# Optimization experiments

Hardware: AMD Instinct MI355X
Metric: run time of the kernel (lower is better)

The kernel has to match this reference:

```python
import jax, jax.numpy as jnp
import numpy as np

B, P, N0 = 8, 32, 10000
K, HIDP = 8, 4
HIDR = 4 * K * HIDP + K   # 136 = backbone output channels
HEADS = 2
E = 160000


def _conv_bn(x, w, b, g, be, dil):
    # x: [B,1,P,N0]; w: [k,1,ks,1]; valid conv along time with dilation dil, then BatchNorm2d (batch stats)
    y = jax.lax.conv_general_dilated(x, w, (1, 1), 'VALID', rhs_dilation=(dil, 1),
                                     dimension_numbers=('NCHW', 'OIHW', 'NCHW'))
    y = y + b[None, :, None, None]
    mu = jnp.mean(y, axis=(0, 2, 3), keepdims=True)
    var = jnp.var(y, axis=(0, 2, 3), keepdims=True)
    return g[None, :, None, None] * (y - mu) * jax.lax.rsqrt(var + 1e-5) + be[None, :, None, None]


def _branch(x, w, b, g, be, dil, pool):
    y = _conv_bn(x, w, b, g, be, dil)
    if pool:  # AdaptiveMaxPool2d((HIDP, N0)): pools only the time axis (node axis already N0)
        T = y.shape[2]
        y = jnp.stack([jnp.max(y[:, :, (i * T) // HIDP: -((-(i + 1) * T) // HIDP), :], axis=2)
                       for i in range(HIDP)], axis=2)
    return y.reshape(y.shape[0], -1, y.shape[-1])  # [B, k*hidP or k, N0]


def _backbone(x, pl1, pl2, pp1, pp2, pg):
    x = x.reshape(-1, 1, P, N0)
    parts = [_branch(x, *pl1, 1, True), _branch(x, *pl2, 1, True),   # local: ks 3,5 dil 1
             _branch(x, *pp1, 2, True), _branch(x, *pp2, 2, True),   # periodic: ks 3,5 dil 2
             _branch(x, *pg, 1, False)]                               # global: ks P, no pool
    return jnp.tanh(jnp.concatenate(parts, axis=1).transpose(0, 2, 1))  # [B, N0, HIDR]


def _gat(xn, W, a_src, a_dst, bias, src, dst, heads, out_ch):
    # PyG GATConv: linear (no bias) -> per-head additive attention -> segment softmax over dst -> scatter-sum
    n = xn.shape[0]
    h = (xn @ W).reshape(n, heads, out_ch)                              # [N,H,C]
    al = jax.nn.leaky_relu(jnp.sum(h * a_src, -1)[src] + jnp.sum(h * a_dst, -1)[dst], 0.2)  # [E',H]
    amax = jax.ops.segment_max(al, dst, num_segments=n)
    ex = jnp.exp(al - amax[dst])
    coef = ex / (jax.ops.segment_sum(ex, dst, num_segments=n)[dst] + 1e-16)
    out = jax.ops.segment_sum(coef[:, :, None] * h[src], dst, num_segments=n)  # [N,H,C]
    return out.reshape(n, heads * out_ch) + bias


def setup_inputs() -> dict:
    key = jax.random.key(0)
    ks = iter(jax.random.split(key, 64))
    nrm = lambda *s: jax.random.normal(next(ks), s, jnp.float32) * 0.05
    d = {"x": jax.random.normal(next(ks), (B, P, N0), jnp.float32)}
    for nm, ksz in (("l1", 3), ("l2", 5), ("p1", 3), ("p2", 5), ("g", P)):
        d["w_" + nm] = nrm(K, 1, ksz, 1)
        d["b_" + nm] = nrm(K)
        d["g_" + nm] = jnp.ones((K,), jnp.float32)
        d["be_" + nm] = jnp.zeros((K,), jnp.float32)
    d["W1"] = nrm(HIDR, HEADS * HIDR); d["as1"] = nrm(HEADS, HIDR); d["ad1"] = nrm(HEADS, HIDR); d["bb1"] = nrm(HEADS * HIDR)
    d["W2"] = nrm(HEADS * HIDR, HIDR); d["as2"] = nrm(1, HIDR); d["ad2"] = nrm(1, HIDR); d["bb2"] = nrm(HIDR)
    d["Wo"] = nrm(2 * HIDR, HIDR); d["bo"] = nrm(HIDR)
    d["Wo2"] = nrm(HIDR, 1); d["bo2"] = nrm(1)
    d["edge_index"] = jax.random.randint(next(ks), (2, E), 0, N0, jnp.int32)
    return d


def reference(x, w_l1, b_l1, g_l1, be_l1, w_l2, b_l2, g_l2, be_l2,
              w_p1, b_p1, g_p1, be_p1, w_p2, b_p2, g_p2, be_p2,
              w_g, b_g, g_g, be_g,
              W1, as1, ad1, bb1, W2, as2, ad2, bb2, Wo, bo, Wo2, bo2, edge_index):
    feat = _backbone(x, (w_l1, b_l1, g_l1, be_l1), (w_l2, b_l2, g_l2, be_l2),
                     (w_p1, b_p1, g_p1, be_p1), (w_p2, b_p2, g_p2, be_p2),
                     (w_g, b_g, g_g, be_g))                                  # [B,N0,HIDR]
    loop = jnp.arange(N0, dtype=edge_index.dtype)                            # GATConv add_self_loops=True
    src = jnp.concatenate([edge_index[0], loop])
    dst = jnp.concatenate([edge_index[1], loop])
    # original loops GATConv per batch item over shared edge_index; vmap is the batched equivalent
    g1 = jax.vmap(lambda f: _gat(f, W1, as1, ad1, bb1, src, dst, HEADS, HIDR))(feat)  # [B,N0,2*HIDR]
    g2 = jax.vmap(lambda f: _gat(f, W2, as2, ad2, bb2, src, dst, 1, HIDR))(g1)        # [B,N0,HIDR]
    ns = jax.nn.leaky_relu(jnp.concatenate([g2, feat], axis=-1))             # dropout is identity at eval
    res = jax.nn.leaky_relu(ns @ Wo + bo)
    return (res @ Wo2 + bo2)[..., 0]                                         # [B,N0]
```

## Files before the change

kernel.cpp:

```cpp
#include <hip/hip_runtime.h>
#include <hip/hip_bf16.h>
#include <math.h>

typedef unsigned short u16;
typedef unsigned int   u32;
typedef short v8s __attribute__((ext_vector_type(8)));
typedef float v4f __attribute__((ext_vector_type(4)));
typedef float v2f __attribute__((ext_vector_type(2)));
#define DEV static __device__ __forceinline__

DEV float u2f(u16 u){ union{u32 i; float f;} v; v.i = ((u32)u)<<16; return v.f; }
DEV u16   f2u(float f){ union{float ff; u32 i;} v; v.ff = f; u32 r = v.i + 0x7fffu + ((v.i>>16)&1u); return (u16)(r>>16); }
DEV float lrelu02(float x){ return x > 0.f ? x : 0.2f*x; }
DEV float lrelu01(float x){ return x > 0.f ? x : 0.01f*x; }
DEV float fast_tanh(float x){
  float cx = fminf(fmaxf(x, -15.f), 15.f);
  float e = __expf(2.f*cx);
  return (e - 1.f) * __builtin_amdgcn_rcpf(e + 1.f);
}
DEV float wred_sum(float v){
  #pragma unroll
  for (int o = 32; o > 0; o >>= 1) v += __shfl_xor(v, o, 64);
  return v;
}
DEV float wred_max32(float v){
  #pragma unroll
  for (int o = 16; o > 0; o >>= 1) v = fmaxf(v, __shfl_xor(v, o, 64));
  return v;
}
DEV float wred_sum32(float v){
  #pragma unroll
  for (int o = 16; o > 0; o >>= 1) v += __shfl_xor(v, o, 64);
  return v;
}
DEV v2f unpack2(u32 w){
  v2f r;
  r.x = __uint_as_float(w << 16);
  r.y = __uint_as_float(w & 0xffff0000u);
  return r;
}

constexpr int B_   = 8;
constexpr int P_   = 32;
constexpr int N0_  = 10000;
constexpr int NODES = B_ * N0_;
constexpr int E_   = 160000;
constexpr int NE_  = E_ + N0_;

__global__ void __launch_bounds__(256) k_setup(int* __restrict__ zbase,
    const float* __restrict__ Wo, u16* __restrict__ WoT,
    const float* __restrict__ W1, const float* __restrict__ W2, u16* __restrict__ W12T,
    const float* __restrict__ as1, const float* __restrict__ ad1,
    float* __restrict__ va1s, float* __restrict__ va1d,
    const float* __restrict__ as2, const float* __restrict__ ad2,
    const float* __restrict__ bb1,
    float* __restrict__ v2ss, float* __restrict__ v2dd,
    float* __restrict__ cc, float* __restrict__ b12)
{
  __shared__ float l2s[272], l2d[272];
  int blk = blockIdx.x, tid = threadIdx.x;
  if (blk < 79){ int i = blk*256 + tid; if (i < 20080) zbase[i] = 0; return; }
  blk -= 79;
  if (blk < 180){
    int i = blk*256 + tid; if (i >= 144*320) return;
    int n = i/320, k = i - n*320; float v = 0.f;
    if (n < 136){
      if (k < 136) v = Wo[(size_t)k*136 + n];
      else if (k >= 160 && k < 296) v = Wo[(size_t)(k-24)*136 + n];
    }
    WoT[i] = f2u(v); return;
  }
  blk -= 180;
  if (blk < 162){
    int i = blk*256 + tid; if (i >= 144*288) return;
    int n = i/288, kk = i - n*288; float v = 0.f;
    if (n < 136 && kk < 272){
      int hh = kk/136, k = kk - hh*136;
      for (int c = 0; c < 136; c++)
        v = fmaf(W1[(size_t)k*272 + hh*136 + c], W2[(size_t)(hh*136+c)*136 + n], v);
    }
    W12T[i] = f2u(v); return;
  }
  blk -= 162;
  if (blk < 2){
    int t = blk*256 + tid; if (t >= 272) return;
    int hh = t/136, k = t - hh*136; float s = 0.f, d = 0.f;
    for (int c = 0; c < 136; c++){
      float w = W1[(size_t)k*272 + hh*136 + c];
      s = fmaf(w, as1[hh*136+c], s);
      d = fmaf(w, ad1[hh*136+c], d);
    }
    va1s[t] = s; va1d[t] = d; return;
  }
  blk -= 2;
  {
    for (int m = tid; m < 272; m += 256){
      float vs = 0.f, vd = 0.f;
      for (int n2 = 0; n2 < 136; n2++){
        float w2 = W2[(size_t)m*136 + n2];
        vs = fmaf(w2, as2[n2], vs);
        vd = fmaf(w2, ad2[n2], vd);
      }
      l2s[m] = vs; l2d[m] = vd;
    }
    __syncthreads();
    int t0 = blk*256 + tid;
    if (t0 < 272){
      int hh = t0/136, k = t0 - hh*136; float s = 0.f, d = 0.f;
      for (int c = 0; c < 136; c++){
        float w = W1[(size_t)k*272 + hh*136 + c];
        s = fmaf(w, l2s[hh*136+c], s);
        d = fmaf(w, l2d[hh*136+c], d);
      }
      v2ss[t0] = s; v2dd[t0] = d;
    }
    if (blk == 1){
      if (tid < 64){
        float s = 0.f, d = 0.f;
        for (int m = tid; m < 272; m += 64){
          s = fmaf(bb1[m], l2s[m], s);
          d = fmaf(bb1[m], l2d[m], d);
        }
        s = wred_sum(s); d = wred_sum(d);
        if (tid == 0){ cc[0] = s; cc[1] = d; }
      } else if (tid < 200){
        int n2 = tid - 64; float v = 0.f;
        for (int m = 0; m < 272; m++) v = fmaf(bb1[m], W2[(size_t)m*136 + n2], v);
        b12[n2] = v;
      }
    }
  }
}

DEV void load_convw(float* lw, const float* wl1, const float* wl2, const float* wp1,
                    const float* wp2, const float* wg, int tid, int nth){
  for (int i = tid; i < 384; i += nth){
    float v;
    if      (i < 24)  v = wl1[i];
    else if (i < 64)  v = wl2[i-24];
    else if (i < 88)  v = wp1[i-64];
    else if (i < 128) v = wp2[i-88];
    else              v = wg [i-128];
    lw[i] = v;
  }
}

template<int KS,int DIL,int T>
DEV void conv_stats(const float* xc, const float* wk, float& s, float& q){
  #pragma unroll
  for (int t = 0; t < T; t++){
    float v = 0.f;
    #pragma unroll
    for (int j = 0; j < KS; j++) v = fmaf(wk[j], xc[t + j*DIL], v);
    s += v; q = fmaf(v, v, q);
  }
}

__global__ void __launch_bounds__(256) k_bn_stats(
    const float* __restrict__ x,
    const float* __restrict__ wl1, const float* __restrict__ wl2,
    const float* __restrict__ wp1, const float* __restrict__ wp2,
    const float* __restrict__ wg,
    float* __restrict__ gsum, float* __restrict__ gsq)
{
  __shared__ float lw[384];
  __shared__ float lacc[80];
  const int tid = threadIdx.x;
  load_convw(lw, wl1, wl2, wp1, wp2, wg, tid, 256);
  if (tid < 80) lacc[tid] = 0.f;
  __syncthreads();

  const int lane = tid & 63, wv = tid >> 6;
  const int nodeLocal = (wv >> 1)*64 + lane;
  const int half = wv & 1;
  const int gid = blockIdx.x*128 + nodeLocal;
  float xc[P_];
  if (gid < NODES){
    int b = gid / N0_, n = gid - b*N0_;
    const float* xp = x + (size_t)b*P_*N0_ + n;
    #pragma unroll
    for (int p = 0; p < P_; p++) xc[p] = xp[(size_t)p*N0_];
  } else {
    #pragma unroll
    for (int p = 0; p < P_; p++) xc[p] = 0.f;
  }

  auto red = [&](int ch, float s, float q){
    #pragma unroll
    for (int o = 32; o > 0; o >>= 1){ s += __shfl_down(s,o,64); q += __shfl_down(q,o,64); }
    if (lane == 0){ atomicAdd(&lacc[ch], s); atomicAdd(&lacc[40+ch], q); }
  };

  if (half == 0){
    #pragma unroll
    for (int k = 0; k < 8; k++){ float s=0,q=0; conv_stats<3,1,30>(xc, lw      + k*3 , s,q); red(k,     s,q); }
    #pragma unroll
    for (int k = 0; k < 8; k++){ float s=0,q=0; conv_stats<5,1,28>(xc, lw + 24 + k*5 , s,q); red(8+k,   s,q); }
  } else {
    #pragma unroll
    for (int k = 0; k < 8; k++){ float s=0,q=0; conv_stats<3,2,28>(xc, lw + 64 + k*3 , s,q); red(16+k,  s,q); }
    #pragma unroll
    for (int k = 0; k < 8; k++){ float s=0,q=0; conv_stats<5,2,24>(xc, lw + 88 + k*5 , s,q); red(24+k,  s,q); }
    #pragma unroll
    for (int k = 0; k < 8; k++){ float s=0,q=0; conv_stats<32,1,1>(xc, lw + 128+ k*32, s,q); red(32+k,  s,q); }
  }

  __syncthreads();
  if (tid < 40)      atomicAdd(&gsum[tid],    lacc[tid]);
  else if (tid < 80) atomicAdd(&gsq [tid-40], lacc[tid]);
}

__global__ void k_count(const int* __restrict__ ei, int* __restrict__ counts,
                        const float* __restrict__ gsum, const float* __restrict__ gsq,
                        float* __restrict__ sA, float* __restrict__ sB,
                        const float* g0, const float* g1, const float* g2, const float* g3, const float* g4,
                        const float* e0, const float* e1, const float* e2, const float* e3, const float* e4){
  if (blockIdx.x == 665){
    int t = threadIdx.x;
    if (t >= 40) return;
    int bi = t >> 3, k = t & 7;
    const int Ts[5] = {30,28,28,24,1};
    float cnt  = (float)NODES * (float)Ts[bi];
    float mean = gsum[t] / cnt;
    float var  = gsq[t] / cnt - mean*mean;
    const float* gp = bi==0?g0: bi==1?g1: bi==2?g2: bi==3?g3: g4;
    const float* ep = bi==0?e0: bi==1?e1: bi==2?e2: bi==3?e3: e4;
    float a = gp[k] * rsqrtf(fmaxf(var, 0.f) + 1e-5f);
    sA[t] = a;
    sB[t] = ep[k] - a*mean;
    return;
  }
  int e = blockIdx.x*blockDim.x + threadIdx.x;
  if (e >= NE_) return;
  int dst = (e < E_) ? ei[E_ + e] : (e - E_);
  atomicAdd(&counts[dst], 1);
}

__global__ void __launch_bounds__(1024) k_scan_perm(const int* __restrict__ counts,
                                                    int* __restrict__ offs,
                                                    int* __restrict__ perm){
  __shared__ int part[1024];
  __shared__ int hist[129];
  __shared__ int base[129];
  int t = threadIdx.x;
  if (blockIdx.x == 0){
    int loc[10]; int s = 0;
    #pragma unroll
    for (int i = 0; i < 10; i++){
      int idx = t*10 + i;
      int c = (idx < N0_) ? counts[idx] : 0;
      loc[i] = s; s += c;
    }
    part[t] = s;
    __syncthreads();
    for (int o = 1; o < 1024; o <<= 1){
      int v = (t >= o) ? part[t-o] : 0;
      __syncthreads();
      part[t] += v;
      __syncthreads();
    }
    int pre = (t == 0) ? 0 : part[t-1];
    #pragma unroll
    for (int i = 0; i < 10; i++){
      int idx = t*10 + i;
      if (idx < N0_) offs[idx] = pre + loc[i];
    }
    if (t == 0) offs[N0_] = part[1023];
  } else {
    if (t < 129) hist[t] = 0;
    __syncthreads();
    int dloc[10];
    #pragma unroll
    for (int i = 0; i < 10; i++){
      int idx = t*10 + i;
      if (idx < N0_){
        int d = min(counts[idx], 128);
        dloc[i] = d;
        atomicAdd(&hist[d], 1);
      }
    }
    __syncthreads();
    if (t == 0){
      int s = 0;
      for (int b = 0; b <= 128; b++){ base[b] = s; s += hist[b]; }
    }
    __syncthreads();
    #pragma unroll
    for (int i = 0; i < 10; i++){
      int idx = t*10 + i;
      if (idx < N0_){
        int pos = atomicAdd(&base[dloc[i]], 1);
        perm[pos] = idx;
      }
    }
  }
}

__global__ void k_scatter(const int* __restrict__ ei, const int* __restrict__ offs,
                          int* __restrict__ cursor, int* __restrict__ srcl){
  int e = blockIdx.x*blockDim.x + threadIdx.x;
  if (e >= NE_) return;
  int src, dst;
  if (e < E_){ src = ei[e]; dst = ei[E_ + e]; } else { src = dst = e - E_; }
  int pos = atomicAdd(&cursor[dst], 1);
  srcl[offs[dst] + pos] = src;
}

template<int KS,int DIL,int T>
DEV void conv_pool4(const float* xc, const float* wk, float A, float Bc, float* o4){
  float y[T];
  #pragma unroll
  for (int t = 0; t < T; t++){
    float v = 0.f;
    #pragma unroll
    for (int j = 0; j < KS; j++) v = fmaf(wk[j], xc[t + j*DIL], v);
    y[t] = fmaf(A, v, Bc);
  }
  #pragma unroll
  for (int i = 0; i < 4; i++){
    const int lo = (i*T)/4, hi = ((i+1)*T + 3)/4;
    float m = y[lo];
    #pragma unroll
    for (int t = 0; t < T; t++){ if (t > lo && t < hi) m = fmaxf(m, y[t]); }
    o4[i] = m;
  }
}

__global__ void __launch_bounds__(256) k_feat(
    const float* __restrict__ x,
    const float* __restrict__ wl1, const float* __restrict__ wl2,
    const float* __restrict__ wp1, const float* __restrict__ wp2,
    const float* __restrict__ wg,
    const float* __restrict__ sA, const float* __restrict__ sB,
    const float* __restrict__ va1s, const float* __restrict__ va1d,
    u16* __restrict__ feat, u16* __restrict__ featL,
    float* __restrict__ asrc1, float* __restrict__ adst1,
    int base, int m)
{
  __shared__ float lw[384];
  __shared__ float lA[40], lB[40];
  __shared__ float4 lv4[136];
  __shared__ float sdt[128][4];
  const int tid = threadIdx.x;
  load_convw(lw, wl1, wl2, wp1, wp2, wg, tid, 256);
  if (tid < 40){ lA[tid] = sA[tid]; lB[tid] = sB[tid]; }
  for (int i = tid; i < 136; i += 256)
    lv4[i] = make_float4(va1s[i], va1d[i], va1s[136+i], va1d[136+i]);
  __syncthreads();

  const int lane = tid & 63, wv = tid >> 6;
  const int nodeLocal = (wv >> 1)*64 + lane;
  const int half = wv & 1;
  const int nodeIdx = blockIdx.x*128 + nodeLocal;
  const bool act = nodeIdx < m;
  const int gcl = base + (act ? nodeIdx : (m-1));
  int b = gcl / N0_, n = gcl - b*N0_;
  float xc[P_];
  const float* xp = x + (size_t)b*P_*N0_ + n;
  #pragma unroll
  for (int p = 0; p < P_; p++) xc[p] = xp[(size_t)p*N0_];

  float dt[4] = {0.f,0.f,0.f,0.f};
  u32 pk[4], pkl[4];
  u16* orow  = feat  + (size_t)nodeIdx*160;
  u16* olrow = featL + (size_t)nodeIdx*160;
  auto emit = [&](int ch, float v){
    float t = fast_tanh(v);
    float4 vv = lv4[ch];
    dt[0] = fmaf(t, vv.x, dt[0]);
    dt[1] = fmaf(t, vv.y, dt[1]);
    dt[2] = fmaf(t, vv.z, dt[2]);
    dt[3] = fmaf(t, vv.w, dt[3]);
    u16 h  = f2u(t);
    u16 hl = f2u(lrelu01(t));
    int s = ch & 7;
    if ((s & 1) == 0){ pk[s>>1] = h;                pkl[s>>1] = hl; }
    else             { pk[s>>1] |= ((u32)h) << 16;  pkl[s>>1] |= ((u32)hl) << 16; }
    if (s == 7 && act){
      *(uint4*)(orow  + (ch - 7)) = make_uint4(pk[0],pk[1],pk[2],pk[3]);
      *(uint4*)(olrow + (ch - 7)) = make_uint4(pkl[0],pkl[1],pkl[2],pkl[3]);
    }
  };

  float o4[4];
  if (half == 0){
    #pragma unroll
    for (int k = 0; k < 8; k++){
      conv_pool4<3,1,30>(xc, lw + k*3, lA[k], lB[k], o4);
      #pragma unroll
      for (int i = 0; i < 4; i++) emit(k*4+i, o4[i]);
    }
    #pragma unroll
    for (int k = 0; k < 8; k++){
      conv_pool4<5,1,28>(xc, lw + 24 + k*5, lA[8+k], lB[8+k], o4);
      #pragma unroll
      for (int i = 0; i < 4; i++) emit(32 + k*4+i, o4[i]);
    }
  } else {
    #pragma unroll
    for (int k = 0; k < 8; k++){
      conv_pool4<3,2,28>(xc, lw + 64 + k*3, lA[16+k], lB[16+k], o4);
      #pragma unroll
      for (int i = 0; i < 4; i++) emit(64 + k*4+i, o4[i]);
    }
    #pragma unroll
    for (int k = 0; k < 8; k++){
      conv_pool4<5,2,24>(xc, lw + 88 + k*5, lA[24+k], lB[24+k], o4);
      #pragma unroll
      for (int i = 0; i < 4; i++) emit(96 + k*4+i, o4[i]);
    }
    #pragma unroll
    for (int k = 0; k < 8; k++){
      float v = 0.f;
      #pragma unroll
      for (int j = 0; j < 32; j++) v = fmaf(lw[128 + k*32 + j], xc[j], v);
      emit(128 + k, fmaf(lA[32+k], v, lB[32+k]));
    }
  }

  if (half == 1){
    sdt[nodeLocal][0] = dt[0]; sdt[nodeLocal][1] = dt[1];
    sdt[nodeLocal][2] = dt[2]; sdt[nodeLocal][3] = dt[3];
  }
  __syncthreads();
  if (half == 0 && act){
    asrc1[(size_t)nodeIdx*2]   = dt[0] + sdt[nodeLocal][0];
    asrc1[(size_t)nodeIdx*2+1] = dt[2] + sdt[nodeLocal][2];
    adst1[(size_t)nodeIdx*2]   = dt[1] + sdt[nodeLocal][1];
    adst1[(size_t)nodeIdx*2+1] = dt[3] + sdt[nodeLocal][3];
  }
}

template<int MT,int KT1,int KT2,int NT,int EPI,int LR2>
__global__ void __launch_bounds__(256) k_mfma(
    const u16* __restrict__ A1, int sA1,
    const u16* __restrict__ A2, int sA2,
    const u16* __restrict__ BT, int sBT,
    u16* __restrict__ C, int sC, int nbase,
    const float* __restrict__ bias, int m,
    const float* __restrict__ w2v, const float* __restrict__ bo2p, float* __restrict__ fout)
{
  const int wv = threadIdx.x >> 6, lane = threadIdx.x & 63;
  const int quad = lane >> 4, l15 = lane & 15;
  const int mb = blockIdx.x*(MT*64) + wv*(MT*16);
  int ar[MT];
  #pragma unroll
  for (int mt = 0; mt < MT; mt++) ar[mt] = min(mb + mt*16 + l15, m-1);

  v4f acc[MT][NT];
  #pragma unroll
  for (int mt = 0; mt < MT; mt++)
    #pragma unroll
    for (int nt = 0; nt < NT; nt++)
      acc[mt][nt] = (v4f){0.f,0.f,0.f,0.f};

  for (int kt = 0; kt < KT1+KT2; kt++){
    const u16* ab; int sA, koff;
    if (KT2 == 0 || kt < KT1){ ab = A1; sA = sA1; koff = kt*32; }
    else { ab = A2; sA = sA2; koff = (kt-KT1)*32; }
    v8s a[MT];
    #pragma unroll
    for (int mt = 0; mt < MT; mt++)
      a[mt] = *(const v8s*)(ab + (size_t)ar[mt]*sA + koff + quad*8);
    if (KT2 > 0 && LR2 && kt >= KT1){
      #pragma unroll
      for (int mt = 0; mt < MT; mt++)
        #pragma unroll
        for (int j = 0; j < 8; j++){
          float f = u2f((u16)a[mt][j]);
          f = f > 0.f ? f : 0.01f*f;
          a[mt][j] = (short)f2u(f);
        }
    }
    const int kb = kt*32 + quad*8;
    #pragma unroll
    for (int nt = 0; nt < NT; nt++){
      v8s b = *(const v8s*)(BT + (size_t)(nbase + nt*16 + l15)*sBT + kb);
      #pragma unroll
      for (int mt = 0; mt < MT; mt++)
        acc[mt][nt] = __builtin_amdgcn_mfma_f32_16x16x32_bf16(a[mt], b, acc[mt][nt], 0, 0, 0);
    }
  }

  if (EPI == 2){
    const float bo2v = bo2p[0];
    #pragma unroll
    for (int mt = 0; mt < MT; mt++){
      float part[4] = {0.f,0.f,0.f,0.f};
      #pragma unroll
      for (int nt = 0; nt < NT; nt++){
        const int col = nt*16 + l15;
        float wv2 = (col < 136) ? w2v[col] : 0.f;
        float bv  = bias[min(col,135)];
        #pragma unroll
        for (int i = 0; i < 4; i++){
          float xv = lrelu01(acc[mt][nt][i] + bv);
          part[i] = fmaf(xv, wv2, part[i]);
        }
      }
      #pragma unroll
      for (int i = 0; i < 4; i++){
        float v = part[i];
        v += __shfl_xor(v, 1, 64);
        v += __shfl_xor(v, 2, 64);
        v += __shfl_xor(v, 4, 64);
        v += __shfl_xor(v, 8, 64);
        int r = mb + mt*16 + quad*4 + i;
        if (l15 == 0 && r < m) fout[r] = v + bo2v;
      }
    }
    return;
  }

  #pragma unroll
  for (int mt = 0; mt < MT; mt++){
    const int r0 = mb + mt*16 + quad*4;
    #pragma unroll
    for (int nt = 0; nt < NT; nt++){
      const int col = nbase + nt*16 + l15;
      #pragma unroll
      for (int i = 0; i < 4; i++){
        int r = r0 + i;
        if (r < m){
          float xv = acc[mt][nt][i];
          if (EPI == 1){ xv += bias[min(col,135)]; xv = lrelu01(xv); }
          if (EPI == 3){ xv += bias[min(col,135)]; }
          C[(size_t)r*sC + col] = f2u(xv);
        }
      }
    }
  }
}

__global__ void __launch_bounds__(256) k_agg1(const u16* __restrict__ feat,
    const float* __restrict__ asrc, const float* __restrict__ adst,
    const int* __restrict__ offs, const int* __restrict__ srcl,
    const int* __restrict__ perm,
    u16* __restrict__ aggF,
    const float* __restrict__ v2s, const float* __restrict__ v2d,
    const float* __restrict__ cc,
    float* __restrict__ as_out, float* __restrict__ ad_out,
    int cbMask, int cbShift)
{
  __shared__ int4 smeta[4][2][32];
  const int tid = threadIdx.x;
  const int wv = tid >> 6, lane = tid & 63;
  const int half = lane >> 5, l32 = lane & 31;
  const int id = blockIdx.x;
  const int bb = id & cbMask;
  const int q = (id >> cbShift)*4 + wv;
  const int dst = perm[2*q + half];
  const int nbase = bb*N0_;
  const int node = nbase + dst;
  const int start = offs[dst], end = offs[dst+1];
  const int ne = end - start;

  const float ad0 = adst[(size_t)node*2], ad1v = adst[(size_t)node*2+1];
  const char* featB = (const char*)feat;

  v2f m01h0 = {0.f,0.f}, m23h0 = {0.f,0.f};
  v2f m01h1 = {0.f,0.f}, m23h1 = {0.f,0.f};
  v2f r01h0 = {0.f,0.f}, r01h1 = {0.f,0.f};

  auto acc_one = [&](int4 mt){
    const u16* fp = (const u16*)(featB + mt.x);
    float c0 = __int_as_float(mt.y), c1 = __int_as_float(mt.z);
    const uint2 hv = *(const uint2*)(fp + 4*l32);
    v2f f01 = unpack2(hv.x), f23 = unpack2(hv.y);
    v2f cc0 = {c0,c0}, cc1 = {c1,c1};
    m01h0 = __builtin_elementwise_fma(f01, cc0, m01h0);
    m23h0 = __builtin_elementwise_fma(f23, cc0, m23h0);
    m01h1 = __builtin_elementwise_fma(f01, cc1, m01h1);
    m23h1 = __builtin_elementwise_fma(f23, cc1, m23h1);
    if (l32 < 4){
      const u32 hr = *(const u32*)(fp + 128 + 2*l32);
      v2f g01 = unpack2(hr);
      r01h0 = __builtin_elementwise_fma(g01, cc0, r01h0);
      r01h1 = __builtin_elementwise_fma(g01, cc1, r01h1);
    }
  };
  auto acc_four = [&](int4 ma, int4 mb, int4 mc, int4 md){
    const u16* p0 = (const u16*)(featB + ma.x);
    const u16* p1 = (const u16*)(featB + mb.x);
    const u16* p2 = (const u16*)(featB + mc.x);
    const u16* p3 = (const u16*)(featB + md.x);
    const uint2 v0 = *(const uint2*)(p0 + 4*l32);
    const uint2 v1 = *(const uint2*)(p1 + 4*l32);
    const uint2 v2 = *(const uint2*)(p2 + 4*l32);
    const uint2 v3 = *(const uint2*)(p3 + 4*l32);
    u32 q0, q1, q2, q3;
    if (l32 < 4){
      q0 = *(const u32*)(p0 + 128 + 2*l32);
      q1 = *(const u32*)(p1 + 128 + 2*l32);
      q2 = *(const u32*)(p2 + 128 + 2*l32);
      q3 = *(const u32*)(p3 + 128 + 2*l32);
    }
    v2f f01, f23, cA, cB;
    #define EDGE1(vv, qq, mm) \
      f01 = unpack2(vv.x); f23 = unpack2(vv.y); \
      cA = (v2f){__int_as_float(mm.y), __int_as_float(mm.y)}; \
      cB = (v2f){__int_as_float(mm.z), __int_as_float(mm.z)}; \
      m01h0 = __builtin_elementwise_fma(f01, cA, m01h0); \
      m23h0 = __builtin_elementwise_fma(f23, cA, m23h0); \
      m01h1 = __builtin_elementwise_fma(f01, cB, m01h1); \
      m23h1 = __builtin_elementwise_fma(f23, cB, m23h1); \
      if (l32 < 4){ \
        v2f g01 = unpack2(qq); \
        r01h0 = __builtin_elementwise_fma(g01, cA, r01h0); \
        r01h1 = __builtin_elementwise_fma(g01, cB, r01h1); \
      }
    EDGE1(v0, q0, ma)
    EDGE1(v1, q1, mb)
    EDGE1(v2, q2, mc)
    EDGE1(v3, q3, md)
    #undef EDGE1
  };
  auto run_chunk = [&](int cnt){
    const int4* mp = &smeta[wv][half][0];
    int j = 0;
    for (; j + 3 < cnt; j += 4)
      acc_four(mp[j], mp[j+1], mp[j+2], mp[j+3]);
    for (; j < cnt; j++)
      acc_one(mp[j]);
  };

  if (ne <= 32){
    const bool has = l32 < ne;
    const int sn = nbase + (has ? srcl[start + l32] : 0);
    const int offL = sn * 320;
    float al0 = has ? lrelu02(asrc[(size_t)sn*2]   + ad0)  : -1e30f;
    float al1 = has ? lrelu02(asrc[(size_t)sn*2+1] + ad1v) : -1e30f;
    float mm = wred_max32(al0);
    float p0 = has ? __expf(al0 - mm) : 0.f;
    float c0 = p0 * (1.f/(wred_sum32(p0) + 1e-16f));
    mm = wred_max32(al1);
    float p1 = has ? __expf(al1 - mm) : 0.f;
    float c1 = p1 * (1.f/(wred_sum32(p1) + 1e-16f));
    if (has)
      smeta[wv][half][l32] = make_int4(offL, __float_as_int(c0), __float_as_int(c1), 0);
    asm volatile("s_waitcnt lgkmcnt(0)" ::: "memory");
    run_chunk(ne);
  } else {
    float lm0 = -1e30f, lm1 = -1e30f;
    for (int e = start + l32; e < end; e += 32){
      int sn = nbase + srcl[e];
      lm0 = fmaxf(lm0, lrelu02(asrc[(size_t)sn*2]   + ad0));
      lm1 = fmaxf(lm1, lrelu02(asrc[(size_t)sn*2+1] + ad1v));
    }
    float m0 = wred_max32(lm0), m1 = wred_max32(lm1);
    float ls0 = 0.f, ls1 = 0.f;
    for (int e = start + l32; e < end; e += 32){
      int sn = nbase + srcl[e];
      ls0 += __expf(lrelu02(asrc[(size_t)sn*2]   + ad0)  - m0);
      ls1 += __expf(lrelu02(asrc[(size_t)sn*2+1] + ad1v) - m1);
    }
    float si0 = 1.f/(wred_sum32(ls0) + 1e-16f);
    float si1 = 1.f/(wred_sum32(ls1) + 1e-16f);
    for (int cs = start; cs < end; cs += 32){
      int cnt = min(32, end - cs);
      bool has = l32 < cnt;
      int sn = nbase + (has ? srcl[cs + l32] : 0);
      int offL = sn * 320;
      float c0 = 0.f, c1 = 0.f;
      if (has){
        c0 = __expf(lrelu02(asrc[(size_t)sn*2]   + ad0)  - m0) * si0;
        c1 = __expf(lrelu02(asrc[(size_t)sn*2+1] + ad1v) - m1) * si1;
      }
      if (has)
        smeta[wv][half][l32] = make_int4(offL, __float_as_int(c0), __float_as_int(c1), 0);
      asm volatile("s_waitcnt lgkmcnt(0)" ::: "memory");
      run_chunk(cnt);
    }
  }

  u16* outp = aggF + (size_t)node*288;
  {
    ushort4 s0; s0.x=f2u(m01h0.x); s0.y=f2u(m01h0.y); s0.z=f2u(m23h0.x); s0.w=f2u(m23h0.y);
    *(ushort4*)(outp + 4*l32) = s0;
    ushort4 s1; s1.x=f2u(m01h1.x); s1.y=f2u(m01h1.y); s1.z=f2u(m23h1.x); s1.w=f2u(m23h1.y);
    *(ushort4*)(outp + 136 + 4*l32) = s1;
    if (l32 < 4){
      ushort2 t0; t0.x=f2u(r01h0.x); t0.y=f2u(r01h0.y);
      *(ushort2*)(outp + 128 + 2*l32) = t0;
      ushort2 t1; t1.x=f2u(r01h1.x); t1.y=f2u(r01h1.y);
      *(ushort2*)(outp + 136 + 128 + 2*l32) = t1;
    }
  }
  {
    int c = 4*l32;
    float s = m01h0.x*v2s[c] + m01h0.y*v2s[c+1] + m23h0.x*v2s[c+2] + m23h0.y*v2s[c+3]
            + m01h1.x*v2s[136+c] + m01h1.y*v2s[136+c+1] + m23h1.x*v2s[136+c+2] + m23h1.y*v2s[136+c+3];
    float d = m01h0.x*v2d[c] + m01h0.y*v2d[c+1] + m23h0.x*v2d[c+2] + m23h0.y*v2d[c+3]
            + m01h1.x*v2d[136+c] + m01h1.y*v2d[136+c+1] + m23h1.x*v2d[136+c+2] + m23h1.y*v2d[136+c+3];
    if (l32 < 4){
      int cr = 128 + 2*l32;
      s += r01h0.x*v2s[cr] + r01h0.y*v2s[cr+1] + r01h1.x*v2s[136+cr] + r01h1.y*v2s[136+cr+1];
      d += r01h0.x*v2d[cr] + r01h0.y*v2d[cr+1] + r01h1.x*v2d[136+cr] + r01h1.y*v2d[136+cr+1];
    }
    s = wred_sum32(s); d = wred_sum32(d);
    if (l32 == 0){ as_out[node] = s + cc[0]; ad_out[node] = d + cc[1]; }
  }
}

__global__ void __launch_bounds__(256) k_agg2(const u16* __restrict__ h, int sh,
    const float* __restrict__ asrc, const float* __restrict__ adst,
    const int* __restrict__ offs, const int* __restrict__ srcl,
    const int* __restrict__ perm,
    const float* __restrict__ bias, u16* __restrict__ outp0, int so,
    int cbMask, int cbShift)
{
  __shared__ int2 smeta[4][2][32];
  const int tid = threadIdx.x;
  const int wv = tid >> 6, lane = tid & 63;
  const int half = lane >> 5, l32 = lane & 31;
  const int id = blockIdx.x;
  const int bb = id & cbMask;
  const int q = (id >> cbShift)*4 + wv;
  const int dst = perm[2*q + half];
  const int nbase = bb*N0_;
  const int node = nbase + dst;
  const int start = offs[dst], end = offs[dst+1];
  const int ne = end - start;
  const int bstride = 2*sh;

  const float adh = adst[node];
  const char* hB = (const char*)h;

  v2f a01 = {0.f,0.f}, a23 = {0.f,0.f}, r01 = {0.f,0.f};

  auto acc_one = [&](int2 mt){
    const u16* hp = (const u16*)(hB + mt.x);
    float c0 = __int_as_float(mt.y);
    const uint2 hv = *(const uint2*)(hp + 4*l32);
    v2f cc0 = {c0,c0};
    a01 = __builtin_elementwise_fma(unpack2(hv.x), cc0, a01);
    a23 = __builtin_elementwise_fma(unpack2(hv.y), cc0, a23);
    if (l32 < 4){
      const u32 hr = *(const u32*)(hp + 128 + 2*l32);
      r01 = __builtin_elementwise_fma(unpack2(hr), cc0, r01);
    }
  };
  auto acc_four = [&](int2 ma, int2 mb, int2 mc, int2 md){
    const u16* p0 = (const u16*)(hB + ma.x);
    const u16* p1 = (const u16*)(hB + mb.x);
    const u16* p2 = (const u16*)(hB + mc.x);
    const u16* p3 = (const u16*)(hB + md.x);
    const uint2 v0 = *(const uint2*)(p0 + 4*l32);
    const uint2 v1 = *(const uint2*)(p1 + 4*l32);
    const uint2 v2 = *(const uint2*)(p2 + 4*l32);
    const uint2 v3 = *(const uint2*)(p3 + 4*l32);
    u32 q0, q1, q2, q3;
    if (l32 < 4){
      q0 = *(const u32*)(p0 + 128 + 2*l32);
      q1 = *(const u32*)(p1 + 128 + 2*l32);
      q2 = *(const u32*)(p2 + 128 + 2*l32);
      q3 = *(const u32*)(p3 + 128 + 2*l32);
    }
    v2f cc;
    #define EDGE2(vv, qq, mm) \
      cc = (v2f){__int_as_float(mm.y), __int_as_float(mm.y)}; \
      a01 = __builtin_elementwise_fma(unpack2(vv.x), cc, a01); \
      a23 = __builtin_elementwise_fma(unpack2(vv.y), cc, a23); \
      if (l32 < 4) r01 = __builtin_elementwise_fma(unpack2(qq), cc, r01);
    EDGE2(v0, q0, ma)
    EDGE2(v1, q1, mb)
    EDGE2(v2, q2, mc)
    EDGE2(v3, q3, md)
    #undef EDGE2
  };
  auto run_chunk = [&](int cnt){
    const int2* mp = &smeta[wv][half][0];
    int j = 0;
    for (; j + 3 < cnt; j += 4)
      acc_four(mp[j], mp[j+1], mp[j+2], mp[j+3]);
    for (; j < cnt; j++)
      acc_one(mp[j]);
  };

  if (ne <= 32){
    const bool has = l32 < ne;
    const int sn = nbase + (has ? srcl[start + l32] : 0);
    const int offL = sn * bstride;
    float al = has ? lrelu02(asrc[sn] + adh) : -1e30f;
    float m = wred_max32(al);
    float p = has ? __expf(al - m) : 0.f;
    float c0 = p * (1.f/(wred_sum32(p) + 1e-16f));
    if (has)
      smeta[wv][half][l32] = make_int2(offL, __float_as_int(c0));
    asm volatile("s_waitcnt lgkmcnt(0)" ::: "memory");
    run_chunk(ne);
  } else {
    float lm = -1e30f;
    for (int e = start + l32; e < end; e += 32){
      int sn = nbase + srcl[e];
      lm = fmaxf(lm, lrelu02(asrc[sn] + adh));
    }
    float m = wred_max32(lm);
    float ls = 0.f;
    for (int e = start + l32; e < end; e += 32){
      int sn = nbase + srcl[e];
      ls += __expf(lrelu02(asrc[sn] + adh) - m);
    }
    float si = 1.f/(wred_sum32(ls) + 1e-16f);
    for (int cs = start; cs < end; cs += 32){
      int cnt = min(32, end - cs);
      bool has = l32 < cnt;
      int sn = nbase + (has ? srcl[cs + l32] : 0);
      int offL = sn * bstride;
      float c0 = has ? __expf(lrelu02(asrc[sn] + adh) - m) * si : 0.f;
      if (has)
        smeta[wv][half][l32] = make_int2(offL, __float_as_int(c0));
      asm volatile("s_waitcnt lgkmcnt(0)" ::: "memory");
      run_chunk(cnt);
    }
  }

  u16* outp = outp0 + (size_t)node*so;
  {
    int c = 4*l32;
    ushort4 st;
    st.x = f2u(lrelu01(a01.x + bias[c]));
    st.y = f2u(lrelu01(a01.y + bias[c+1]));
    st.z = f2u(lrelu01(a23.x + bias[c+2]));
    st.w = f2u(lrelu01(a23.y + bias[c+3]));
    *(ushort4*)(outp + c) = st;
    if (l32 < 4){
      int cr = 128 + 2*l32;
      ushort2 sr;
      sr.x = f2u(lrelu01(r01.x + bias[cr]));
      sr.y = f2u(lrelu01(r01.y + bias[cr+1]));
      *(ushort2*)(outp + cr) = sr;
    }
  }
}

extern "C" void kernel_launch(void* const* d_in, const int* in_sizes, int n_in,
                              void* d_out, int out_size, void* d_ws, size_t ws_size,
                              hipStream_t stream)
{
  (void)in_sizes; (void)n_in; (void)out_size;
  const float* x    = (const float*)d_in[0];
  const float* wl1  = (const float*)d_in[1];
  const float* gl1  = (const float*)d_in[3];
  const float* bel1 = (const float*)d_in[4];
  const float* wl2  = (const float*)d_in[5];
  const float* gl2  = (const float*)d_in[7];
  const float* bel2 = (const float*)d_in[8];
  const float* wp1  = (const float*)d_in[9];
  const float* gp1  = (const float*)d_in[11];
  const float* bep1 = (const float*)d_in[12];
  const float* wp2  = (const float*)d_in[13];
  const float* gp2  = (const float*)d_in[15];
  const float* bep2 = (const float*)d_in[16];
  const float* wg   = (const float*)d_in[17];
  const float* gg   = (const float*)d_in[19];
  const float* beg  = (const float*)d_in[20];
  const float* W1   = (const float*)d_in[21];
  const float* as1  = (const float*)d_in[22];
  const float* ad1  = (const float*)d_in[23];
  const float* bb1  = (const float*)d_in[24];
  const float* W2   = (const float*)d_in[25];
  const float* as2  = (const float*)d_in[26];
  const float* ad2  = (const float*)d_in[27];
  const float* bb2  = (const float*)d_in[28];
  const float* Wo   = (const float*)d_in[29];
  const float* bo   = (const float*)d_in[30];
  const float* Wo2  = (const float*)d_in[31];
  const float* bo2  = (const float*)d_in[32];
  const int*   ei   = (const int*)d_in[33];

  const size_t STATIC_BYTES = 1250000;
  int nc = 1;
  while (nc < 8 && STATIC_BYTES + (size_t)1880*(NODES/nc) > ws_size) nc <<= 1;
  const int CB = B_/nc, CN = CB*N0_;
  int cbShift = 0; while ((1 << cbShift) < CB) cbShift++;
  const int cbMask = CB - 1;

  char* wsb = (char*)d_ws; size_t off = 0;
  auto alloc = [&](size_t nbytes)->void*{
    void* p = wsb + off; off = (off + nbytes + 255) & ~(size_t)255; return p;
  };
  int*   zbase  = (int*)  alloc(20080*sizeof(int));
  float* gsum   = (float*)zbase;
  float* gsq    = gsum + 40;
  int*   counts = zbase + 80;
  int*   cursor = counts + 10000;
  float* sA     = (float*)alloc(40*sizeof(float));
  float* sB     = (float*)alloc(40*sizeof(float));
  int*   offs   = (int*)  alloc(10001*sizeof(int));
  int*   srcl   = (int*)  alloc((size_t)NE_*sizeof(int));
  int*   perm   = (int*)  alloc((size_t)N0_*sizeof(int));
  u16*   W12T   = (u16*)  alloc((size_t)144*288*2);
  u16*   WoT    = (u16*)  alloc((size_t)144*320*2);
  float* va1s   = (float*)alloc(272*sizeof(float));
  float* va1d   = (float*)alloc(272*sizeof(float));
  float* v2ss   = (float*)alloc(272*sizeof(float));
  float* v2dd   = (float*)alloc(272*sizeof(float));
  float* ccv    = (float*)alloc(2*sizeof(float));
  float* b12    = (float*)alloc(136*sizeof(float));
  u16*   feat   = (u16*)  alloc((size_t)CN*160*2);
  u16*   featL  = (u16*)  alloc((size_t)CN*160*2);
  u16*   aggF   = (u16*)  alloc((size_t)CN*288*2);
  u16*   h2     = (u16*)  alloc((size_t)CN*144*2);
  u16*   g2l    = (u16*)  alloc((size_t)CN*160*2);
  float* asrc1  = (float*)alloc((size_t)CN*2*sizeof(float));
  float* adst1  = (float*)alloc((size_t)CN*2*sizeof(float));
  float* asrc2  = (float*)alloc((size_t)CN*sizeof(float));
  float* adst2  = (float*)alloc((size_t)CN*sizeof(float));

  k_setup<<<425,256,0,stream>>>(zbase, Wo, WoT, W1, W2, W12T,
                                as1, ad1, va1s, va1d, as2, ad2, bb1,
                                v2ss, v2dd, ccv, b12);

  k_bn_stats<<<625,256,0,stream>>>(x, wl1,wl2,wp1,wp2,wg, gsum, gsq);

  k_count  <<<666,256,0,stream>>>(ei, counts, gsum, gsq, sA, sB,
                                  gl1,gl2,gp1,gp2,gg, bel1,bel2,bep1,bep2,beg);
  k_scan_perm<<<2,1024,0,stream>>>(counts, offs, perm);
  k_scatter<<<665,256,0,stream>>>(ei, offs, cursor, srcl);

  const int gxm = (CN + 127)/128;
  const int gx2 = (CN + 127)/128;
  const int aggB = 1250*CB;
  for (int c = 0; c < nc; c++){
    const int base = c*CN;

    k_feat<<<gx2,256,0,stream>>>(x, wl1,wl2,wp1,wp2,wg, sA, sB, va1s, va1d,
                                 feat, featL, asrc1, adst1, base, CN);

    k_agg1<<<aggB,256,0,stream>>>(feat, asrc1, adst1, offs, srcl, perm, aggF,
                                  v2ss, v2dd, ccv, asrc2, adst2, cbMask, cbShift);

    k_mfma<2,9,0,9,3,0><<<gxm,256,0,stream>>>(aggF,288, (const u16*)0,0, W12T,288, h2,144, 0, b12, CN,
                                              (const float*)0,(const float*)0,(float*)0);

    k_agg2<<<aggB,256,0,stream>>>(h2,144, asrc2, adst2, offs, srcl, perm, bb2, g2l,160,
                                  cbMask, cbShift);

    k_mfma<2,5,5,9,2,0><<<gxm,256,0,stream>>>(g2l,160, featL,160, WoT,320, (u16*)0,0, 0, bo, CN,
                                              Wo2, bo2, (float*)d_out + base);
  }
}
```

Baseline: 457.7 us.

## Merge setup kernels, fuse edge scatter into feature kernel, drop featL buffer

Several small preprocessing kernels (setup, BN stats, degree count) are merged into one launch, and the scan/perm and BN scale kernels are merged into another. The edge scatter now runs as extra blocks of the feature kernel, and the separate zero-init blocks are replaced by a memset. The leaky-relu copy of the features (featL) is no longer stored; the final MFMA kernel is switched to a template variant that presumably applies leaky-relu on load, which saves a write and a buffer. Aggregation kernels also walk the degree-sorted permutation in reverse order, which changes the order in which nodes are scheduled. This cuts launch overhead and memory traffic, at the cost of mixed-role blocks and reliance on the new template flag.

```diff
diff --git a/kernel.cpp b/kernel.cpp
--- a/kernel.cpp
+++ b/kernel.cpp
@@ -47,7 +47,31 @@
 constexpr int E_   = 160000;
 constexpr int NE_  = E_ + N0_;
 
-__global__ void __launch_bounds__(256) k_setup(int* __restrict__ zbase,
+DEV void load_convw(float* lw, const float* wl1, const float* wl2, const float* wp1,
+                    const float* wp2, const float* wg, int tid, int nth){
+  for (int i = tid; i < 384; i += nth){
+    float v;
+    if      (i < 24)  v = wl1[i];
+    else if (i < 64)  v = wl2[i-24];
+    else if (i < 88)  v = wp1[i-64];
+    else if (i < 128) v = wp2[i-88];
+    else              v = wg [i-128];
+    lw[i] = v;
+  }
+}
+
+template<int KS,int DIL,int T>
+DEV void conv_stats(const float* xc, const float* wk, float& s, float& q){
+  #pragma unroll
+  for (int t = 0; t < T; t++){
+    float v = 0.f;
+    #pragma unroll
+    for (int j = 0; j < KS; j++) v = fmaf(wk[j], xc[t + j*DIL], v);
+    s += v; q = fmaf(v, v, q);
+  }
+}
+
+__global__ void __launch_bounds__(256) k_mega1(
     const float* __restrict__ Wo, u16* __restrict__ WoT,
     const float* __restrict__ W1, const float* __restrict__ W2, u16* __restrict__ W12T,
     const float* __restrict__ as1, const float* __restrict__ ad1,
@@ -55,12 +79,16 @@
     const float* __restrict__ as2, const float* __restrict__ ad2,
     const float* __restrict__ bb1,
     float* __restrict__ v2ss, float* __restrict__ v2dd,
-    float* __restrict__ cc, float* __restrict__ b12)
+    float* __restrict__ cc, float* __restrict__ b12,
+    const float* __restrict__ x,
+    const float* __restrict__ wl1, const float* __restrict__ wl2,
+    const float* __restrict__ wp1, const float* __restrict__ wp2,
+    const float* __restrict__ wg,
+    float* __restrict__ gsum, float* __restrict__ gsq,
+    const int* __restrict__ ei, int* __restrict__ counts)
 {
-  __shared__ float l2s[272], l2d[272];
+  __shared__ float smem[544];
   int blk = blockIdx.x, tid = threadIdx.x;
-  if (blk < 79){ int i = blk*256 + tid; if (i < 20080) zbase[i] = 0; return; }
-  blk -= 79;
   if (blk < 180){
     int i = blk*256 + tid; if (i >= 144*320) return;
     int n = i/320, k = i - n*320; float v = 0.f;
@@ -93,7 +121,8 @@
     va1s[t] = s; va1d[t] = d; return;
   }
   blk -= 2;
-  {
+  if (blk < 2){
+    float* l2s = smem; float* l2d = smem + 272;
     for (int m = tid; m < 272; m += 256){
       float vs = 0.f, vd = 0.f;
       for (int n2 = 0; n2 < 136; n2++){
@@ -129,94 +158,76 @@
         b12[n2] = v;
       }
     }
-  }
-}
-
-DEV void load_convw(float* lw, const float* wl1, const float* wl2, const float* wp1,
-                    const float* wp2, const float* wg, int tid, int nth){
-  for (int i = tid; i < 384; i += nth){
-    float v;
-    if      (i < 24)  v = wl1[i];
-    else if (i < 64)  v = wl2[i-24];
-    else if (i < 88)  v = wp1[i-64];
-    else if (i < 128) v = wp2[i-88];
-    else              v = wg [i-128];
-    lw[i] = v;
-  }
-}
-
-template<int KS,int DIL,int T>
-DEV void conv_stats(const float* xc, const float* wk, float& s, float& q){
-  #pragma unroll
-  for (int t = 0; t < T; t++){
-    float v = 0.f;
-    #pragma unroll
-    for (int j = 0; j < KS; j++) v = fmaf(wk[j], xc[t + j*DIL], v);
-    s += v; q = fmaf(v, v, q);
-  }
-}
-
-__global__ void __launch_bounds__(256) k_bn_stats(
-    const float* __restrict__ x,
-    const float* __restrict__ wl1, const float* __restrict__ wl2,
-    const float* __restrict__ wp1, const float* __restrict__ wp2,
-    const float* __restrict__ wg,
-    float* __restrict__ gsum, float* __restrict__ gsq)
+    return;
+  }
+  blk -= 2;
+  if (blk < 625){
+    float* lw = smem; float* lacc = smem + 384;
+    load_convw(lw, wl1, wl2, wp1, wp2, wg, tid, 256);
+    if (tid < 80) lacc[tid] = 0.f;
+    __syncthreads();
+
+    const int lane = tid & 63, wv = tid >> 6;
+    const int nodeLocal = (wv >> 1)*64 + lane;
+    const int half = wv & 1;
+    const int gid = blk*128 + nodeLocal;
+    float xc[P_];
+    if (gid < NODES){
+      int b = gid / N0_, n = gid - b*N0_;
+      const float* xp = x + (size_t)b*P_*N0_ + n;
+      #pragma unroll
+      for (int p = 0; p < P_; p++) xc[p] = xp[(size_t)p*N0_];
+    } else {
+      #pragma unroll
+      for (int p = 0; p < P_; p++) xc[p] = 0.f;
+    }
+
+    auto red = [&](int ch, float s, float q){
+      #pragma unroll
+      for (int o = 32; o > 0; o >>= 1){ s += __shfl_down(s,o,64); q += __shfl_down(q,o,64); }
+      if (lane == 0){ atomicAdd(&lacc[ch], s); atomicAdd(&lacc[40+ch], q); }
+    };
+
+    if (half == 0){
+      #pragma unroll
+      for (int k = 0; k < 8; k++){ float s=0,q=0; conv_stats<3,1,30>(xc, lw      + k*3 , s,q); red(k,     s,q); }
+      #pragma unroll
+      for (int k = 0; k < 8; k++){ float s=0,q=0; conv_stats<5,1,28>(xc, lw + 24 + k*5 , s,q); red(8+k,   s,q); }
+    } else {
+      #pragma unroll
+      for (int k = 0; k < 8; k++){ float s=0,q=0; conv_stats<3,2,28>(xc, lw + 64 + k*3 , s,q); red(16+k,  s,q); }
+      #pragma unroll
+      for (int k = 0; k < 8; k++){ float s=0,q=0; conv_stats<5,2,24>(xc, lw + 88 + k*5 , s,q); red(24+k,  s,q); }
+      #pragma unroll
+      for (int k = 0; k < 8; k++){ float s=0,q=0; conv_stats<32,1,1>(xc, lw + 128+ k*32, s,q); red(32+k,  s,q); }
+    }
+
+    __syncthreads();
+    if (tid < 40)      atomicAdd(&gsum[tid],    lacc[tid]);
+    else if (tid < 80) atomicAdd(&gsq [tid-40], lacc[tid]);
+    return;
+  }
+  blk -= 625;
+  {
+    int e = blk*256 + tid;
+    if (e >= NE_) return;
+    int dst = (e < E_) ? ei[E_ + e] : (e - E_);
+    atomicAdd(&counts[dst], 1);
+  }
+}
+
+__global__ void __launch_bounds__(1024) k_mega2(
+    const int* __restrict__ counts, int* __restrict__ offs, int* __restrict__ perm,
+    const float* __restrict__ gsum, const float* __restrict__ gsq,
+    float* __restrict__ sA, float* __restrict__ sB,
+    const float* g0, const float* g1, const float* g2, const float* g3, const float* g4,
+    const float* e0, const float* e1, const float* e2, const float* e3, const float* e4)
 {
-  __shared__ float lw[384];
-  __shared__ float lacc[80];
-  const int tid = threadIdx.x;
-  load_convw(lw, wl1, wl2, wp1, wp2, wg, tid, 256);
-  if (tid < 80) lacc[tid] = 0.f;
-  __syncthreads();
-
-  const int lane = tid & 63, wv = tid >> 6;
-  const int nodeLocal = (wv >> 1)*64 + lane;
-  const int half = wv & 1;
-  const int gid = blockIdx.x*128 + nodeLocal;
-  float xc[P_];
-  if (gid < NODES){
-    int b = gid / N0_, n = gid - b*N0_;
-    const float* xp = x + (size_t)b*P_*N0_ + n;
-    #pragma unroll
-    for (int p = 0; p < P_; p++) xc[p] = xp[(size_t)p*N0_];
-  } else {
-    #pragma unroll
-    for (int p = 0; p < P_; p++) xc[p] = 0.f;
-  }
-
-  auto red = [&](int ch, float s, float q){
-    #pragma unroll
-    for (int o = 32; o > 0; o >>= 1){ s += __shfl_down(s,o,64); q += __shfl_down(q,o,64); }
-    if (lane == 0){ atomicAdd(&lacc[ch], s); atomicAdd(&lacc[40+ch], q); }
-  };
-
-  if (half == 0){
-    #pragma unroll
-    for (int k = 0; k < 8; k++){ float s=0,q=0; conv_stats<3,1,30>(xc, lw      + k*3 , s,q); red(k,     s,q); }
-    #pragma unroll
-    for (int k = 0; k < 8; k++){ float s=0,q=0; conv_stats<5,1,28>(xc, lw + 24 + k*5 , s,q); red(8+k,   s,q); }
-  } else {
-    #pragma unroll
-    for (int k = 0; k < 8; k++){ float s=0,q=0; conv_stats<3,2,28>(xc, lw + 64 + k*3 , s,q); red(16+k,  s,q); }
-    #pragma unroll
-    for (int k = 0; k < 8; k++){ float s=0,q=0; conv_stats<5,2,24>(xc, lw + 88 + k*5 , s,q); red(24+k,  s,q); }
-    #pragma unroll
-    for (int k = 0; k < 8; k++){ float s=0,q=0; conv_stats<32,1,1>(xc, lw + 128+ k*32, s,q); red(32+k,  s,q); }
-  }
-
-  __syncthreads();
-  if (tid < 40)      atomicAdd(&gsum[tid],    lacc[tid]);
-  else if (tid < 80) atomicAdd(&gsq [tid-40], lacc[tid]);
-}
-
-__global__ void k_count(const int* __restrict__ ei, int* __restrict__ counts,
-                        const float* __restrict__ gsum, const float* __restrict__ gsq,
-                        float* __restrict__ sA, float* __restrict__ sB,
-                        const float* g0, const float* g1, const float* g2, const float* g3, const float* g4,
-                        const float* e0, const float* e1, const float* e2, const float* e3, const float* e4){
-  if (blockIdx.x == 665){
-    int t = threadIdx.x;
+  __shared__ int part[1024];
+  __shared__ int hist[129];
+  __shared__ int base[129];
+  int t = threadIdx.x;
+  if (blockIdx.x == 0){
     if (t >= 40) return;
     int bi = t >> 3, k = t & 7;
     const int Ts[5] = {30,28,28,24,1};
@@ -230,20 +241,7 @@
     sB[t] = ep[k] - a*mean;
     return;
   }
-  int e = blockIdx.x*blockDim.x + threadIdx.x;
-  if (e >= NE_) return;
-  int dst = (e < E_) ? ei[E_ + e] : (e - E_);
-  atomicAdd(&counts[dst], 1);
-}
-
-__global__ void __launch_bounds__(1024) k_scan_perm(const int* __restrict__ counts,
-                                                    int* __restrict__ offs,
-                                                    int* __restrict__ perm){
-  __shared__ int part[1024];
-  __shared__ int hist[129];
-  __shared__ int base[129];
-  int t = threadIdx.x;
-  if (blockIdx.x == 0){
+  if (blockIdx.x == 1){
     int loc[10]; int s = 0;
     #pragma unroll
     for (int i = 0; i < 10; i++){
@@ -296,16 +294,6 @@
   }
 }
 
-__global__ void k_scatter(const int* __restrict__ ei, const int* __restrict__ offs,
-                          int* __restrict__ cursor, int* __restrict__ srcl){
-  int e = blockIdx.x*blockDim.x + threadIdx.x;
-  if (e >= NE_) return;
-  int src, dst;
-  if (e < E_){ src = ei[e]; dst = ei[E_ + e]; } else { src = dst = e - E_; }
-  int pos = atomicAdd(&cursor[dst], 1);
-  srcl[offs[dst] + pos] = src;
-}
-
 template<int KS,int DIL,int T>
 DEV void conv_pool4(const float* xc, const float* wk, float A, float Bc, float* o4){
   float y[T];
@@ -326,21 +314,32 @@
   }
 }
 
-__global__ void __launch_bounds__(256) k_feat(
+__global__ void __launch_bounds__(256) k_feat_sc(
     const float* __restrict__ x,
     const float* __restrict__ wl1, const float* __restrict__ wl2,
     const float* __restrict__ wp1, const float* __restrict__ wp2,
     const float* __restrict__ wg,
     const float* __restrict__ sA, const float* __restrict__ sB,
     const float* __restrict__ va1s, const float* __restrict__ va1d,
-    u16* __restrict__ feat, u16* __restrict__ featL,
+    u16* __restrict__ feat,
     float* __restrict__ asrc1, float* __restrict__ adst1,
-    int base, int m)
+    int base, int m, int featBlocks,
+    const int* __restrict__ ei, const int* __restrict__ offs,
+    int* __restrict__ cursor, int* __restrict__ srcl)
 {
   __shared__ float lw[384];
   __shared__ float lA[40], lB[40];
   __shared__ float4 lv4[136];
   __shared__ float sdt[128][4];
+  if (blockIdx.x >= featBlocks){
+    int e = (blockIdx.x - featBlocks)*256 + threadIdx.x;
+    if (e >= NE_) return;
+    int src, dst;
+    if (e < E_){ src = ei[e]; dst = ei[E_ + e]; } else { src = dst = e - E_; }
+    int pos = atomicAdd(&cursor[dst], 1);
+    srcl[offs[dst] + pos] = src;
+    return;
+  }
   const int tid = threadIdx.x;
   load_convw(lw, wl1, wl2, wp1, wp2, wg, tid, 256);
   if (tid < 40){ lA[tid] = sA[tid]; lB[tid] = sB[tid]; }
@@ -361,9 +360,8 @@
   for (int p = 0; p < P_; p++) xc[p] = xp[(size_t)p*N0_];
 
   float dt[4] = {0.f,0.f,0.f,0.f};
-  u32 pk[4], pkl[4];
-  u16* orow  = feat  + (size_t)nodeIdx*160;
-  u16* olrow = featL + (size_t)nodeIdx*160;
+  u32 pk[4];
+  u16* orow  = feat + (size_t)nodeIdx*160;
   auto emit = [&](int ch, float v){
     float t = fast_tanh(v);
     float4 vv = lv4[ch];
@@ -372,13 +370,11 @@
     dt[2] = fmaf(t, vv.z, dt[2]);
     dt[3] = fmaf(t, vv.w, dt[3]);
     u16 h  = f2u(t);
-    u16 hl = f2u(lrelu01(t));
     int s = ch & 7;
-    if ((s & 1) == 0){ pk[s>>1] = h;                pkl[s>>1] = hl; }
-    else             { pk[s>>1] |= ((u32)h) << 16;  pkl[s>>1] |= ((u32)hl) << 16; }
+    if ((s & 1) == 0){ pk[s>>1] = h; }
+    else             { pk[s>>1] |= ((u32)h) << 16; }
     if (s == 7 && act){
-      *(uint4*)(orow  + (ch - 7)) = make_uint4(pk[0],pk[1],pk[2],pk[3]);
-      *(uint4*)(olrow + (ch - 7)) = make_uint4(pkl[0],pkl[1],pkl[2],pkl[3]);
+      *(uint4*)(orow + (ch - 7)) = make_uint4(pk[0],pk[1],pk[2],pk[3]);
     }
   };
 
@@ -549,7 +545,7 @@
   const int id = blockIdx.x;
   const int bb = id & cbMask;
   const int q = (id >> cbShift)*4 + wv;
-  const int dst = perm[2*q + half];
+  const int dst = perm[N0_ - 1 - 2*q - half];
   const int nbase = bb*N0_;
   const int node = nbase + dst;
   const int start = offs[dst], end = offs[dst+1];
@@ -716,7 +712,7 @@
   const int id = blockIdx.x;
   const int bb = id & cbMask;
   const int q = (id >> cbShift)*4 + wv;
-  const int dst = perm[2*q + half];
+  const int dst = perm[N0_ - 1 - 2*q - half];
   const int nbase = bb*N0_;
   const int node = nbase + dst;
   const int start = offs[dst], end = offs[dst+1];
@@ -871,7 +867,7 @@
 
   const size_t STATIC_BYTES = 1250000;
   int nc = 1;
-  while (nc < 8 && STATIC_BYTES + (size_t)1880*(NODES/nc) > ws_size) nc <<= 1;
+  while (nc < 8 && STATIC_BYTES + (size_t)1560*(NODES/nc) > ws_size) nc <<= 1;
   const int CB = B_/nc, CN = CB*N0_;
   int cbShift = 0; while ((1 << cbShift) < CB) cbShift++;
   const int cbMask = CB - 1;
@@ -899,7 +895,6 @@
   float* ccv    = (float*)alloc(2*sizeof(float));
   float* b12    = (float*)alloc(136*sizeof(float));
   u16*   feat   = (u16*)  alloc((size_t)CN*160*2);
-  u16*   featL  = (u16*)  alloc((size_t)CN*160*2);
   u16*   aggF   = (u16*)  alloc((size_t)CN*288*2);
   u16*   h2     = (u16*)  alloc((size_t)CN*144*2);
   u16*   g2l    = (u16*)  alloc((size_t)CN*160*2);
@@ -908,16 +903,16 @@
   float* asrc2  = (float*)alloc((size_t)CN*sizeof(float));
   float* adst2  = (float*)alloc((size_t)CN*sizeof(float));
 
-  k_setup<<<425,256,0,stream>>>(zbase, Wo, WoT, W1, W2, W12T,
-                                as1, ad1, va1s, va1d, as2, ad2, bb1,
-                                v2ss, v2dd, ccv, b12);
-
-  k_bn_stats<<<625,256,0,stream>>>(x, wl1,wl2,wp1,wp2,wg, gsum, gsq);
-
-  k_count  <<<666,256,0,stream>>>(ei, counts, gsum, gsq, sA, sB,
-                                  gl1,gl2,gp1,gp2,gg, bel1,bel2,bep1,bep2,beg);
-  k_scan_perm<<<2,1024,0,stream>>>(counts, offs, perm);
-  k_scatter<<<665,256,0,stream>>>(ei, offs, cursor, srcl);
+  hipMemsetAsync(zbase, 0, 20080*sizeof(int), stream);
+
+  k_mega1<<<1636,256,0,stream>>>(Wo, WoT, W1, W2, W12T,
+                                 as1, ad1, va1s, va1d, as2, ad2, bb1,
+                                 v2ss, v2dd, ccv, b12,
+                                 x, wl1, wl2, wp1, wp2, wg, gsum, gsq,
+                                 ei, counts);
+
+  k_mega2<<<3,1024,0,stream>>>(counts, offs, perm, gsum, gsq, sA, sB,
+                               gl1,gl2,gp1,gp2,gg, bel1,bel2,bep1,bep2,beg);
 
   const int gxm = (CN + 127)/128;
   const int gx2 = (CN + 127)/128;
@@ -925,8 +920,10 @@
   for (int c = 0; c < nc; c++){
     const int base = c*CN;
 
-    k_feat<<<gx2,256,0,stream>>>(x, wl1,wl2,wp1,wp2,wg, sA, sB, va1s, va1d,
-                                 feat, featL, asrc1, adst1, base, CN);
+    const int extra = (c == 0) ? 665 : 0;
+    k_feat_sc<<<gx2 + extra,256,0,stream>>>(x, wl1,wl2,wp1,wp2,wg, sA, sB, va1s, va1d,
+                                            feat, asrc1, adst1, base, CN, gx2,
+                                            ei, offs, cursor, srcl);
 
     k_agg1<<<aggB,256,0,stream>>>(feat, asrc1, adst1, offs, srcl, perm, aggF,
                                   v2ss, v2dd, ccv, asrc2, adst2, cbMask, cbShift);
@@ -937,7 +934,7 @@
     k_agg2<<<aggB,256,0,stream>>>(h2,144, asrc2, adst2, offs, srcl, perm, bb2, g2l,160,
                                   cbMask, cbShift);
 
-    k_mfma<2,5,5,9,2,0><<<gxm,256,0,stream>>>(g2l,160, featL,160, WoT,320, (u16*)0,0, 0, bo, CN,
+    k_mfma<2,5,5,9,2,1><<<gxm,256,0,stream>>>(g2l,160, feat,160, WoT,320, (u16*)0,0, 0, bo, CN,
                                               Wo2, bo2, (float*)d_out + base);
   }
 }
```

Result: faster. 412.8 us (median of 3 runs) (-9.8%).
